# Performance work log

Hardware: AMD Instinct MI355X
Metric: run time of the kernel (lower is better)

## Reference

```python
import jax, jax.numpy as jnp
import numpy as np

B, Q, C = 8, 100, 1024
H, W = 64, 64
NH = 16
HD = C // NH
SCALE = HD ** -0.5
LN_EPS = 1e-5


def setup_inputs() -> dict:
    key = jax.random.key(0)
    ks = jax.random.split(key, 8)
    xav = lambda k, shp: jax.random.normal(k, shp, jnp.float32) * (2.0 / (shp[0] + shp[-1])) ** 0.5
    return {
        "tgt": jax.random.normal(ks[0], (B, Q, C), jnp.float32),
        "memory": jax.random.normal(ks[1], (B, H, W, C), jnp.float32),
        "memory_pos_emb": jax.random.normal(ks[2], (B, H, W, C), jnp.float32),
        "query_pos_emb": jax.random.normal(ks[3], (B, Q, C), jnp.float32),
        "Wq": xav(ks[4], (C, C)),
        "Wk": xav(ks[5], (C, C)),
        "Wv": xav(ks[6], (C, C)),
        "Wo": xav(ks[7], (C, C)),
        "bo": jnp.zeros((C,), jnp.float32),
        "ln_gamma": jnp.ones((C,), jnp.float32),
        "ln_beta": jnp.zeros((C,), jnp.float32),
    }


def _layernorm(x, g, b):
    mu = jnp.mean(x, axis=-1, keepdims=True)
    var = jnp.var(x, axis=-1, keepdims=True)
    return (x - mu) * jax.lax.rsqrt(var + LN_EPS) * g + b


def reference(tgt, memory, memory_pos_emb, query_pos_emb, Wq, Wk, Wv, Wo, bo, ln_gamma, ln_beta):
    # flatten spatial dims: [B,H,W,C] -> [B,K,C]
    mem = memory.reshape(B, H * W, C)
    mpos = memory_pos_emb.reshape(B, H * W, C)
    q_in = tgt + query_pos_emb          # [B,Q,C]
    k_in = mem + mpos                    # [B,K,C]
    # projections (torch Linear: x @ W.T), split heads -> [B,nh,*,hd]
    q = (q_in @ Wq.T).reshape(B, Q, NH, HD).transpose(0, 2, 1, 3)
    k = (k_in @ Wk.T).reshape(B, -1, NH, HD).transpose(0, 2, 1, 3)
    v = (mem @ Wv.T).reshape(B, -1, NH, HD).transpose(0, 2, 1, 3)
    dots = jnp.einsum('bhid,bhjd->bhij', q, k) * SCALE   # [B,nh,Q,K]
    # slot attention: softmax over QUERY axis, then renormalize over keys
    attn = jax.nn.softmax(dots, axis=2)
    attn = attn / (jnp.sum(attn, axis=-1, keepdims=True) + 1e-8)
    updates = jnp.einsum('bhij,bhjd->bhid', attn, v)     # [B,nh,Q,hd]
    updates = updates.transpose(0, 2, 1, 3).reshape(B, Q, C)
    out = updates @ Wo.T + bo
    # residual (dropout is identity in eval) + post-LayerNorm
    return _layernorm(tgt + out, ln_gamma, ln_beta)
```

## Files before the change

kernel.cpp:

```cpp
#include <hip/hip_runtime.h>

typedef unsigned short u16;
typedef __attribute__((ext_vector_type(8))) short bf16x8;
typedef __attribute__((ext_vector_type(4))) short bf16x4;
typedef __attribute__((ext_vector_type(4))) float f32x4;
typedef __attribute__((ext_vector_type(4))) unsigned short u16x4;
typedef __attribute__((ext_vector_type(8))) unsigned short u16x8;
typedef __attribute__((ext_vector_type(4))) int i32x4;
typedef __attribute__((ext_vector_type(4))) float f4;

#define DI __device__ __forceinline__


DI u16 f2bf(float f){
  unsigned int u = __float_as_uint(f);
  return (u16)((u + 0x7FFFu + ((u >> 16) & 1u)) >> 16);
}

DI void gl_lds16(const void* g, void* l){
  __builtin_amdgcn_global_load_lds((const __attribute__((address_space(1))) unsigned int*)g,
                                   (__attribute__((address_space(3))) unsigned int*)l, 16, 0, 0);
}

__global__ __launch_bounds__(256) void prep_kv(const float* __restrict__ mem,
                                               const float* __restrict__ mpos,
                                               u16* __restrict__ kA, u16* __restrict__ vA){
  const int t = blockIdx.x * 256 + threadIdx.x;
  #pragma unroll
  for (int i = 0; i < 4; ++i){
    const size_t g = (size_t)t + (size_t)i * 1048576;
    f4 m0 = __builtin_nontemporal_load((const f4*)mem  + g * 2);
    f4 m1 = __builtin_nontemporal_load((const f4*)mem  + g * 2 + 1);
    f4 p0 = __builtin_nontemporal_load((const f4*)mpos + g * 2);
    f4 p1 = __builtin_nontemporal_load((const f4*)mpos + g * 2 + 1);
    u16x8 k, v;
    #pragma unroll
    for (int j = 0; j < 4; ++j){
      k[j]     = f2bf(m0[j] + p0[j]);  v[j]     = f2bf(m0[j]);
      k[j + 4] = f2bf(m1[j] + p1[j]);  v[j + 4] = f2bf(m1[j]);
    }
    ((u16x8*)kA)[g] = k;
    ((u16x8*)vA)[g] = v;
  }
}

__global__ __launch_bounds__(256) void prep_qw(const float* __restrict__ tgt,
                                               const float* __restrict__ qpos,
                                               const float* __restrict__ Wq, const float* __restrict__ Wk,
                                               const float* __restrict__ Wv, const float* __restrict__ Wo,
                                               u16* __restrict__ qA, u16* __restrict__ Wbf){
  int gid = blockIdx.x * 256 + threadIdx.x;
  const int NQ4 = 819200 / 4;
  if (gid < NQ4){
    f4 a = ((const f4*)tgt)[gid];
    f4 b = ((const f4*)qpos)[gid];
    u16x4 r;
    #pragma unroll
    for (int j = 0; j < 4; ++j) r[j] = f2bf(a[j] + b[j]);
    ((u16x4*)qA)[gid] = r;
  } else {
    int wid = gid - NQ4;
    int sel = wid >> 18;
    int off = wid & 262143;
    const float* W = (sel == 0) ? Wq : (sel == 1) ? Wk : (sel == 2) ? Wv : Wo;
    f4 w = ((const f4*)W)[off];
    u16x4 r;
    #pragma unroll
    for (int j = 0; j < 4; ++j) r[j] = f2bf(w[j]);
    ((u16x4*)(Wbf))[(size_t)sel * 262144 + off] = r;
  }
}

__global__ __launch_bounds__(512, 1) void gemm256(
    const u16* __restrict__ A, const u16* __restrict__ Bw,
    u16* __restrict__ Cb, float scale)
{
  __shared__ __align__(16) char lds[131072];
  const int tid = threadIdx.x;
  const int l = tid & 63, w = tid >> 6;
  const int nwg = gridDim.x;
  const int sbid = (blockIdx.x & 7) * (nwg >> 3) + (blockIdx.x >> 3);
  const int mb = sbid >> 2, nb = sbid & 3;
  const int m0 = mb * 256, n0 = nb * 256;
  const int fr = l & 15, fg = l >> 4;
  const int wm = w >> 2, wn = w & 3;

  char* ldsA  = lds + wm * 8192 + l * 16;
  char* ldsB  = lds + 32768 + wn * 4096 + l * 16;
  char* ldsS0 = lds + w * 1024;
  char* ldsS1 = lds + (8 + w) * 1024;
  const u16* gA0 = A  + (size_t)(m0 + w * 16 + fr) * 1024 + fg * 8;
  const u16* gA1 = A  + (size_t)(m0 + (8 + w) * 16 + fr) * 1024 + fg * 8;
  const u16* gB0 = Bw + (size_t)(n0 + w * 16 + fr) * 1024 + fg * 8;
  const u16* gB1 = Bw + (size_t)(n0 + (8 + w) * 16 + fr) * 1024 + fg * 8;

  auto stA = [&](int pp, int kh, int kt){
    const int o = kt * 64 + kh * 32;
    gl_lds16(gA0 + o, ldsS0 + pp * 65536 + kh * 16384);
    gl_lds16(gA1 + o, ldsS1 + pp * 65536 + kh * 16384);
  };
  auto stB = [&](int pp, int kh, int kt){
    const int o = kt * 64 + kh * 32;
    gl_lds16(gB0 + o, ldsS0 + pp * 65536 + 32768 + kh * 16384);
    gl_lds16(gB1 + o, ldsS1 + pp * 65536 + 32768 + kh * 16384);
  };
  auto rdA4 = [&](bf16x8* av, int pp, int kh, int mfb){
    #pragma unroll
    for (int i = 0; i < 4; ++i)
      av[i] = *(const bf16x8*)(ldsA + pp * 65536 + kh * 16384 + (mfb + i) * 1024);
  };
  auto rdB4 = [&](bf16x8* bv, int pp, int kh){
    #pragma unroll
    for (int i = 0; i < 4; ++i)
      bv[i] = *(const bf16x8*)(ldsB + pp * 65536 + kh * 16384 + i * 1024);
  };

  f32x4 acc[8][4] = {};

  stA(0, 0, 0); stB(0, 0, 0); stA(0, 1, 0); stB(0, 1, 0);
  stA(1, 0, 1); stB(1, 0, 1);
  asm volatile("s_waitcnt vmcnt(8)" ::: "memory");
  __builtin_amdgcn_s_barrier();

  auto ktbody = [&](int P, int kt){
    const int kt1 = (kt + 1 > 15) ? 15 : kt + 1;
    const int kt2 = (kt + 2 > 15) ? 15 : kt + 2;
    bf16x8 av[4], bv[4];

    rdA4(av, P, 0, 0); rdB4(bv, P, 0);
    stA(P ^ 1, 1, kt1);
    __builtin_amdgcn_s_barrier();
    __builtin_amdgcn_s_setprio(1);
    #pragma unroll
    for (int i = 0; i < 4; ++i)
      #pragma unroll
      for (int n = 0; n < 4; ++n)
        acc[i][n] = __builtin_amdgcn_mfma_f32_16x16x32_bf16(av[i], bv[n], acc[i][n], 0, 0, 0);
    __builtin_amdgcn_s_setprio(0);
    __builtin_amdgcn_s_barrier();

    rdA4(av, P, 0, 4);
    stB(P ^ 1, 1, kt1);
    asm volatile("s_waitcnt vmcnt(8)" ::: "memory");
    __builtin_amdgcn_s_barrier();
    __builtin_amdgcn_s_setprio(1);
    #pragma unroll
    for (int i = 0; i < 4; ++i)
      #pragma unroll
      for (int n = 0; n < 4; ++n)
        acc[4 + i][n] = __builtin_amdgcn_mfma_f32_16x16x32_bf16(av[i], bv[n], acc[4 + i][n], 0, 0, 0);
    __builtin_amdgcn_s_setprio(0);
    __builtin_amdgcn_s_barrier();

    rdA4(av, P, 1, 0); rdB4(bv, P, 1);
    stA(P, 0, kt2);
    __builtin_amdgcn_s_barrier();
    __builtin_amdgcn_s_setprio(1);
    #pragma unroll
    for (int i = 0; i < 4; ++i)
      #pragma unroll
      for (int n = 0; n < 4; ++n)
        acc[i][n] = __builtin_amdgcn_mfma_f32_16x16x32_bf16(av[i], bv[n], acc[i][n], 0, 0, 0);
    __builtin_amdgcn_s_setprio(0);
    __builtin_amdgcn_s_barrier();

    rdA4(av, P, 1, 4);
    stB(P, 0, kt2);
    asm volatile("s_waitcnt vmcnt(8)" ::: "memory");
    __builtin_amdgcn_s_barrier();
    __builtin_amdgcn_s_setprio(1);
    #pragma unroll
    for (int i = 0; i < 4; ++i)
      #pragma unroll
      for (int n = 0; n < 4; ++n)
        acc[4 + i][n] = __builtin_amdgcn_mfma_f32_16x16x32_bf16(av[i], bv[n], acc[4 + i][n], 0, 0, 0);
    __builtin_amdgcn_s_setprio(0);
    __builtin_amdgcn_s_barrier();
  };

  for (int kk = 0; kk < 8; ++kk){
    ktbody(0, 2 * kk);
    ktbody(1, 2 * kk + 1);
  }

  asm volatile("s_waitcnt vmcnt(0)" ::: "memory");

  #pragma unroll
  for (int mf = 0; mf < 8; ++mf){
    #pragma unroll
    for (int nf = 0; nf < 4; ++nf){
      const int gcol = n0 + wn * 64 + nf * 16 + fr;
      #pragma unroll
      for (int r = 0; r < 4; ++r){
        const int grow = m0 + wm * 128 + mf * 16 + fg * 4 + r;
        Cb[(size_t)grow * 1024 + gcol] = f2bf(acc[mf][nf][r] * scale);
      }
    }
  }
}

template<int MODE>
__global__ __launch_bounds__(256, 2) void gemm_bt(
    const u16* __restrict__ A, const u16* __restrict__ Bw,
    u16* __restrict__ Cb, float* __restrict__ Cf,
    const float* __restrict__ bias, const float* __restrict__ resid,
    int M, float scale)
{
  __shared__ u16 lA[2][128 * 32];
  __shared__ u16 lB[2][128 * 32];
  const int tid = threadIdx.x;
  const int l = tid & 63, w = tid >> 6;
  const int nwg = gridDim.x;
  int bid = blockIdx.x;
  bid = (bid & 7) * (nwg >> 3) + (bid >> 3);
  const int mb = bid >> 3, nb = bid & 7;
  const int m0 = mb * 128, n0 = nb * 128;
  const int fr = l & 15, fg = l >> 4;
  const int wr = w >> 1, wc = w & 1;

  f32x4 acc[4][4] = {};

  auto stage = [&](int buf, int kt){
    const int k0 = kt * 32;
    #pragma unroll
    for (int q = 0; q < 2; ++q){
      int r = w * 32 + q * 16 + (l >> 2);
      int ar = m0 + r; if (ar >= M) ar = M - 1;
      gl_lds16(A  + (size_t)ar * 1024 + k0 + (l & 3) * 8, &lA[buf][(w * 32 + q * 16) * 32]);
      gl_lds16(Bw + (size_t)(n0 + r) * 1024 + k0 + (l & 3) * 8, &lB[buf][(w * 32 + q * 16) * 32]);
    }
  };

  stage(0, 0);
  __syncthreads();
  for (int kt = 0; kt < 32; ++kt){
    const int cur = kt & 1;
    if (kt < 31) stage(cur ^ 1, kt + 1);
    bf16x8 av[4], bv[4];
    #pragma unroll
    for (int m = 0; m < 4; ++m)
      av[m] = *(const bf16x8*)&lA[cur][(wr * 64 + m * 16 + fr) * 32 + fg * 8];
    #pragma unroll
    for (int n = 0; n < 4; ++n)
      bv[n] = *(const bf16x8*)&lB[cur][(wc * 64 + n * 16 + fr) * 32 + fg * 8];
    #pragma unroll
    for (int m = 0; m < 4; ++m)
      #pragma unroll
      for (int n = 0; n < 4; ++n)
        acc[m][n] = __builtin_amdgcn_mfma_f32_16x16x32_bf16(av[m], bv[n], acc[m][n], 0, 0, 0);
    __syncthreads();
  }

  #pragma unroll
  for (int m = 0; m < 4; ++m){
    const int grow_base = m0 + wr * 64 + m * 16 + fg * 4;
    #pragma unroll
    for (int n = 0; n < 4; ++n){
      const int gcol = n0 + wc * 64 + n * 16 + fr;
      #pragma unroll
      for (int r = 0; r < 4; ++r){
        const int grow = grow_base + r;
        if (grow < M){
          const float v = acc[m][n][r];
          if (MODE == 0) Cb[(size_t)grow * 1024 + gcol] = f2bf(v * scale);
          else           Cf[(size_t)grow * 1024 + gcol] = v + bias[gcol] + resid[(size_t)grow * 1024 + gcol];
        }
      }
    }
  }
}

__global__ __launch_bounds__(64, 1) void attn_k(
    const u16* __restrict__ qp, const u16* __restrict__ kp, const u16* __restrict__ vp,
    float* __restrict__ updpart, float* __restrict__ rspart)
{
  const int bidx = blockIdx.x;
  const int c = bidx & 7, h = (bidx >> 3) & 15, b = bidx >> 7;
  const int bh = b * 16 + h;
  const int l = threadIdx.x;
  const int fr = l & 15, fg = l >> 4;

  __shared__ u16 qlds[112 * 64];
  __shared__ __align__(16) u16 vlds[2][16 * 64];

  for (int t = 0; t < 14; ++t){
    int chunk = t * 64 + l;
    int row = chunk >> 3, cb = chunk & 7;
    i32x4 val = {0, 0, 0, 0};
    if (row < 100)
      val = *(const i32x4*)(qp + (size_t)(b * 100 + row) * 1024 + h * 64 + cb * 8);
    *(i32x4*)((char*)qlds + row * 128 + ((cb ^ (row & 7)) * 16)) = val;
  }
  __syncthreads();

  bf16x8 qf[7][2];
  #pragma unroll
  for (int n = 0; n < 7; ++n)
    #pragma unroll
    for (int ks = 0; ks < 2; ++ks){
      int row = n * 16 + fr;
      int cb = ks * 4 + fg;
      qf[n][ks] = *(const bf16x8*)((const char*)qlds + row * 128 + ((cb ^ (row & 7)) * 16));
    }

  f32x4 acc[7][4] = {};
  float rs[7] = {};
  const f32x4 fz = {0.f, 0.f, 0.f, 0.f};
  const size_t kvbase = ((size_t)b * 4096) * 1024 + h * 64;
  const int j00 = c * 512;

  const u16* ksrc = kp + kvbase + (size_t)fr * 1024 + fg * 8;
  const u16* vsrc = vp + kvbase + (size_t)(l >> 3) * 1024 + (l & 7) * 8;

  auto loadK = [&](int t, bf16x8& k0, bf16x8& k1){
    const size_t ro = (size_t)(j00 + t * 16) * 1024;
    k0 = *(const bf16x8*)(ksrc + ro);
    k1 = *(const bf16x8*)(ksrc + ro + 32);
  };
  auto loadV = [&](int t, bf16x8& a, bf16x8& bb){
    const size_t ro = (size_t)(j00 + t * 16) * 1024;
    a  = *(const bf16x8*)(vsrc + ro);
    bb = *(const bf16x8*)(vsrc + ro + 8 * 1024);
  };
  auto writeV = [&](int buf, bf16x8 a, bf16x8 bb){
    *(bf16x8*)&vlds[buf][l * 8] = a;
    *(bf16x8*)&vlds[buf][512 + l * 8] = bb;
  };

  bf16x8 kc0, kc1, kn0, kn1, vn0, vn1;
  loadK(0, kc0, kc1);
  loadV(0, vn0, vn1);
  writeV(0, vn0, vn1);

  for (int t = 0; t < 32; ++t){
    const int cur = t & 1;
    if (t < 31){
      loadK(t + 1, kn0, kn1);
      loadV(t + 1, vn0, vn1);
    }

    f32x4 s[7];
    #pragma unroll
    for (int n = 0; n < 7; ++n){
      s[n] = __builtin_amdgcn_mfma_f32_16x16x32_bf16(kc0, qf[n][0], fz, 0, 0, 0);
      s[n] = __builtin_amdgcn_mfma_f32_16x16x32_bf16(kc1, qf[n][1], s[n], 0, 0, 0);
    }
    if (fr >= 4){ s[6][0] = -1e30f; s[6][1] = -1e30f; s[6][2] = -1e30f; s[6][3] = -1e30f; }

    float pv[7][4];
    #pragma unroll
    for (int r = 0; r < 4; ++r){
      float m = s[0][r];
      #pragma unroll
      for (int n = 1; n < 7; ++n) m = fmaxf(m, s[n][r]);
      m = fmaxf(m, __shfl_xor(m, 1)); m = fmaxf(m, __shfl_xor(m, 2));
      m = fmaxf(m, __shfl_xor(m, 4)); m = fmaxf(m, __shfl_xor(m, 8));
      float sum = 0.f;
      #pragma unroll
      for (int n = 0; n < 7; ++n){ float e = __expf(s[n][r] - m); pv[n][r] = e; sum += e; }
      sum += __shfl_xor(sum, 1); sum += __shfl_xor(sum, 2);
      sum += __shfl_xor(sum, 4); sum += __shfl_xor(sum, 8);
      float inv = 1.0f / sum;
      #pragma unroll
      for (int n = 0; n < 7; ++n) pv[n][r] *= inv;
    }

    bf16x4 pk[7];
    #pragma unroll
    for (int n = 0; n < 7; ++n){
      rs[n] += pv[n][0] + pv[n][1] + pv[n][2] + pv[n][3];
      bf16x4 t4;
      t4[0] = (short)f2bf(pv[n][0]); t4[1] = (short)f2bf(pv[n][1]);
      t4[2] = (short)f2bf(pv[n][2]); t4[3] = (short)f2bf(pv[n][3]);
      pk[n] = t4;
    }

    bf16x4 vf[4];
    #pragma unroll
    for (int dt = 0; dt < 4; ++dt){
      bf16x4 tv;
      #pragma unroll
      for (int jj = 0; jj < 4; ++jj)
        tv[jj] = (short)vlds[cur][(fg * 4 + jj) * 64 + dt * 16 + fr];
      vf[dt] = tv;
    }

    #pragma unroll
    for (int n = 0; n < 7; ++n)
      #pragma unroll
      for (int dt = 0; dt < 4; ++dt)
        acc[n][dt] = __builtin_amdgcn_mfma_f32_16x16x16bf16_1k(vf[dt], pk[n], acc[n][dt], 0, 0, 0);

    if (t < 31){
      writeV(cur ^ 1, vn0, vn1);
      kc0 = kn0; kc1 = kn1;
    }
  }

  #pragma unroll
  for (int n = 0; n < 7; ++n){
    float v = rs[n];
    v += __shfl_xor(v, 16); v += __shfl_xor(v, 32);
    if (l < 16) rspart[((size_t)c * 128 + bh) * 112 + n * 16 + l] = v;
  }
  float* ub = updpart + ((size_t)c * 128 + bh) * 64 * 112;
  #pragma unroll
  for (int n = 0; n < 7; ++n)
    #pragma unroll
    for (int dt = 0; dt < 4; ++dt)
      #pragma unroll
      for (int r = 0; r < 4; ++r){
        int d = dt * 16 + fg * 4 + r;
        int i = n * 16 + fr;
        ub[d * 112 + i] = acc[n][dt][r];
      }
}

__global__ __launch_bounds__(128) void nrm_k(const float* __restrict__ updpart,
                                             const float* __restrict__ rspart,
                                             u16* __restrict__ updn){
  const int bid = blockIdx.x;
  const int d = bid & 63, h = (bid >> 6) & 15, b = bid >> 10;
  const int bh = b * 16 + h;
  const int tid = threadIdx.x;
  const int i = (tid < 112) ? tid : 111;
  float sum = 0.f, rsum = 0.f;
  #pragma unroll
  for (int cc = 0; cc < 8; ++cc){
    sum  += updpart[(((size_t)cc * 128 + bh) * 64 + d) * 112 + i];
    rsum += rspart[((size_t)cc * 128 + bh) * 112 + i];
  }
  if (tid < 100)
    updn[((size_t)b * 100 + tid) * 1024 + h * 64 + d] = f2bf(sum / (rsum + 1e-8f));
}

__global__ __launch_bounds__(256) void ln_k(const float* __restrict__ x,
                                            const float* __restrict__ g,
                                            const float* __restrict__ be,
                                            float* __restrict__ out){
  const int row = blockIdx.x;
  const int tid = threadIdx.x;
  const f4 xv = *(const f4*)(x + (size_t)row * 1024 + tid * 4);
  float s = xv[0] + xv[1] + xv[2] + xv[3];
  float q = xv[0]*xv[0] + xv[1]*xv[1] + xv[2]*xv[2] + xv[3]*xv[3];
  #pragma unroll
  for (int m = 1; m < 64; m <<= 1){ s += __shfl_xor(s, m); q += __shfl_xor(q, m); }
  __shared__ float ss[4], qq[4];
  const int w = tid >> 6;
  if ((tid & 63) == 0){ ss[w] = s; qq[w] = q; }
  __syncthreads();
  s = ss[0] + ss[1] + ss[2] + ss[3];
  q = qq[0] + qq[1] + qq[2] + qq[3];
  const float mu = s * (1.0f / 1024.0f);
  const float var = q * (1.0f / 1024.0f) - mu * mu;
  const float rstd = rsqrtf(var + 1e-5f);
  const f4 gv = *(const f4*)(g + tid * 4);
  const f4 bv = *(const f4*)(be + tid * 4);
  f4 o;
  #pragma unroll
  for (int j = 0; j < 4; ++j) o[j] = (xv[j] - mu) * rstd * gv[j] + bv[j];
  *(f4*)(out + (size_t)row * 1024 + tid * 4) = o;
}

extern "C" void kernel_launch(void* const* d_in, const int* in_sizes, int n_in,
                              void* d_out, int out_size, void* d_ws, size_t ws_size,
                              hipStream_t stream)
{
  const float* tgt   = (const float*)d_in[0];
  const float* mem   = (const float*)d_in[1];
  const float* mpos  = (const float*)d_in[2];
  const float* qpos  = (const float*)d_in[3];
  const float* Wq    = (const float*)d_in[4];
  const float* Wk    = (const float*)d_in[5];
  const float* Wv    = (const float*)d_in[6];
  const float* Wo    = (const float*)d_in[7];
  const float* bo    = (const float*)d_in[8];
  const float* gamma = (const float*)d_in[9];
  const float* beta  = (const float*)d_in[10];

  char* ws = (char*)d_ws;
  u16* qA     = (u16*)(ws + 0);
  u16* Wbf    = (u16*)(ws + 1638400);
  u16* kA     = (u16*)(ws + 10027008);
  u16* vA     = (u16*)(ws + 77135872);
  u16* qproj  = (u16*)(ws + 144244736);
  u16* kproj  = (u16*)(ws + 145883136);
  u16* vproj  = kA;
  float* updpart = (float*)(ws + 77135872);
  float* rspart  = (float*)(ws + 77135872 + 29360128);
  u16*   updn    = (u16*)  (ws + 77135872 + 29818880);
  float* resid   = (float*)(ws + 77135872 + 31457280);

  prep_kv<<<4096, 256, 0, stream>>>(mem, mpos, kA, vA);
  prep_qw<<<4896, 256, 0, stream>>>(tgt, qpos, Wq, Wk, Wv, Wo, qA, Wbf);
  gemm_bt<0><<<56,  256, 0, stream>>>(qA, Wbf, qproj, nullptr, nullptr, nullptr, 800, 0.125f);
  gemm256<<<512, 512, 0, stream>>>(kA, Wbf + 1048576, kproj, 1.0f);
  gemm256<<<512, 512, 0, stream>>>(vA, Wbf + 2097152, vproj, 1.0f);
  attn_k<<<1024, 64, 0, stream>>>(qproj, kproj, vproj, updpart, rspart);
  nrm_k<<<8192, 128, 0, stream>>>(updpart, rspart, updn);
  gemm_bt<1><<<56, 256, 0, stream>>>(updn, Wbf + 3145728, nullptr, resid, bo, tgt, 800, 1.0f);
  ln_k<<<800, 256, 0, stream>>>(resid, gamma, beta, (float*)d_out);
}
```

Measured before the change: 369.7 us.

## Merge K/V projection GEMMs into one launch and split attention keys across two waves

```diff
diff --git a/kernel.cpp b/kernel.cpp
--- a/kernel.cpp
+++ b/kernel.cpp
@@ -71,15 +71,10 @@
   }
 }
 
-__global__ __launch_bounds__(512, 1) void gemm256(
-    const u16* __restrict__ A, const u16* __restrict__ Bw,
-    u16* __restrict__ Cb, float scale)
+DI void gemm256_body(const u16* __restrict__ A, const u16* __restrict__ Bw,
+                     u16* __restrict__ Cb, float scale, int sbid, int tid, char* lds)
 {
-  __shared__ __align__(16) char lds[131072];
-  const int tid = threadIdx.x;
   const int l = tid & 63, w = tid >> 6;
-  const int nwg = gridDim.x;
-  const int sbid = (blockIdx.x & 7) * (nwg >> 3) + (blockIdx.x >> 3);
   const int mb = sbid >> 2, nb = sbid & 3;
   const int m0 = mb * 256, n0 = nb * 256;
   const int fr = l & 15, fg = l >> 4;
@@ -197,6 +192,27 @@
       }
     }
   }
+}
+
+__global__ __launch_bounds__(512, 1) void gemm256(
+    const u16* __restrict__ A, const u16* __restrict__ Bw, u16* __restrict__ Cb)
+{
+  __shared__ __align__(16) char lds[131072];
+  const int nwg = gridDim.x;
+  const int sbid = (blockIdx.x & 7) * (nwg >> 3) + (blockIdx.x >> 3);
+  gemm256_body(A, Bw, Cb, 1.0f, sbid, threadIdx.x, lds);
+}
+
+__global__ __launch_bounds__(512, 1) void gemm256kv(
+    const u16* __restrict__ A0, const u16* __restrict__ B0, u16* __restrict__ C0,
+    const u16* __restrict__ A1, const u16* __restrict__ B1, u16* __restrict__ C1)
+{
+  __shared__ __align__(16) char lds[131072];
+  const int sel = blockIdx.x >> 9;
+  const int inner = blockIdx.x & 511;
+  const int sbid = (inner & 7) * 64 + (inner >> 3);
+  if (sel == 0) gemm256_body(A0, B0, C0, 1.0f, sbid, threadIdx.x, lds);
+  else          gemm256_body(A1, B1, C1, 1.0f, sbid, threadIdx.x, lds);
 }
 
 template<int MODE>
@@ -270,21 +286,25 @@
   }
 }
 
-__global__ __launch_bounds__(64, 1) void attn_k(
+__global__ __launch_bounds__(128, 1) void attn_k(
     const u16* __restrict__ qp, const u16* __restrict__ kp, const u16* __restrict__ vp,
     float* __restrict__ updpart, float* __restrict__ rspart)
 {
   const int bidx = blockIdx.x;
   const int c = bidx & 7, h = (bidx >> 3) & 15, b = bidx >> 7;
   const int bh = b * 16 + h;
-  const int l = threadIdx.x;
+  const int tid = threadIdx.x;
+  const int w = tid >> 6, l = tid & 63;
   const int fr = l & 15, fg = l >> 4;
 
-  __shared__ u16 qlds[112 * 64];
-  __shared__ __align__(16) u16 vlds[2][16 * 64];
-
-  for (int t = 0; t < 14; ++t){
-    int chunk = t * 64 + l;
+  __shared__ __align__(16) char smem[36864];
+  u16*   qlds   = (u16*)smem;
+  f32x4* mrgacc = (f32x4*)smem;
+  u16*   vlds   = (u16*)(smem + 28672);
+  float* mrgrs  = (float*)(smem + 28672);
+
+  for (int t = 0; t < 7; ++t){
+    int chunk = t * 128 + tid;
     int row = chunk >> 3, cb = chunk & 7;
     i32x4 val = {0, 0, 0, 0};
     if (row < 100)
@@ -311,6 +331,7 @@
 
   const u16* ksrc = kp + kvbase + (size_t)fr * 1024 + fg * 8;
   const u16* vsrc = vp + kvbase + (size_t)(l >> 3) * 1024 + (l & 7) * 8;
+  u16* myvlds = vlds + w * 2048;
 
   auto loadK = [&](int t, bf16x8& k0, bf16x8& k1){
     const size_t ro = (size_t)(j00 + t * 16) * 1024;
@@ -323,20 +344,21 @@
     bb = *(const bf16x8*)(vsrc + ro + 8 * 1024);
   };
   auto writeV = [&](int buf, bf16x8 a, bf16x8 bb){
-    *(bf16x8*)&vlds[buf][l * 8] = a;
-    *(bf16x8*)&vlds[buf][512 + l * 8] = bb;
+    *(bf16x8*)&myvlds[buf * 1024 + l * 8] = a;
+    *(bf16x8*)&myvlds[buf * 1024 + 512 + l * 8] = bb;
   };
 
   bf16x8 kc0, kc1, kn0, kn1, vn0, vn1;
-  loadK(0, kc0, kc1);
-  loadV(0, vn0, vn1);
+  loadK(w, kc0, kc1);
+  loadV(w, vn0, vn1);
   writeV(0, vn0, vn1);
 
-  for (int t = 0; t < 32; ++t){
-    const int cur = t & 1;
-    if (t < 31){
-      loadK(t + 1, kn0, kn1);
-      loadV(t + 1, vn0, vn1);
+  for (int tt = 0; tt < 16; ++tt){
+    const int t = 2 * tt + w;
+    const int cur = tt & 1;
+    if (tt < 15){
+      loadK(t + 2, kn0, kn1);
+      loadV(t + 2, vn0, vn1);
     }
 
     f32x4 s[7];
@@ -381,7 +403,7 @@
       bf16x4 tv;
       #pragma unroll
       for (int jj = 0; jj < 4; ++jj)
-        tv[jj] = (short)vlds[cur][(fg * 4 + jj) * 64 + dt * 16 + fr];
+        tv[jj] = (short)myvlds[cur * 1024 + (fg * 4 + jj) * 64 + dt * 16 + fr];
       vf[dt] = tv;
     }
 
@@ -391,29 +413,53 @@
       for (int dt = 0; dt < 4; ++dt)
         acc[n][dt] = __builtin_amdgcn_mfma_f32_16x16x16bf16_1k(vf[dt], pk[n], acc[n][dt], 0, 0, 0);
 
-    if (t < 31){
+    if (tt < 15){
       writeV(cur ^ 1, vn0, vn1);
       kc0 = kn0; kc1 = kn1;
     }
   }
 
+  float rv[7];
   #pragma unroll
   for (int n = 0; n < 7; ++n){
     float v = rs[n];
     v += __shfl_xor(v, 16); v += __shfl_xor(v, 32);
-    if (l < 16) rspart[((size_t)c * 128 + bh) * 112 + n * 16 + l] = v;
-  }
-  float* ub = updpart + ((size_t)c * 128 + bh) * 64 * 112;
-  #pragma unroll
-  for (int n = 0; n < 7; ++n)
-    #pragma unroll
-    for (int dt = 0; dt < 4; ++dt)
-      #pragma unroll
-      for (int r = 0; r < 4; ++r){
-        int d = dt * 16 + fg * 4 + r;
-        int i = n * 16 + fr;
-        ub[d * 112 + i] = acc[n][dt][r];
-      }
+    rv[n] = v;
+  }
+
+  __syncthreads();
+  if (w == 1){
+    #pragma unroll
+    for (int n = 0; n < 7; ++n)
+      #pragma unroll
+      for (int dt = 0; dt < 4; ++dt)
+        mrgacc[(n * 4 + dt) * 64 + l] = acc[n][dt];
+    #pragma unroll
+    for (int n = 0; n < 7; ++n)
+      if (l < 16) mrgrs[n * 16 + l] = rv[n];
+  }
+  __syncthreads();
+  if (w == 0){
+    #pragma unroll
+    for (int n = 0; n < 7; ++n)
+      #pragma unroll
+      for (int dt = 0; dt < 4; ++dt)
+        acc[n][dt] += mrgacc[(n * 4 + dt) * 64 + l];
+    #pragma unroll
+    for (int n = 0; n < 7; ++n)
+      if (l < 16) rspart[((size_t)c * 128 + bh) * 112 + n * 16 + l] = rv[n] + mrgrs[n * 16 + l];
+    float* ub = updpart + ((size_t)c * 128 + bh) * 64 * 112;
+    #pragma unroll
+    for (int n = 0; n < 7; ++n)
+      #pragma unroll
+      for (int dt = 0; dt < 4; ++dt)
+        #pragma unroll
+        for (int r = 0; r < 4; ++r){
+          int d = dt * 16 + fg * 4 + r;
+          int i = n * 16 + fr;
+          ub[d * 112 + i] = acc[n][dt][r];
+        }
+  }
 }
 
 __global__ __launch_bounds__(128) void nrm_k(const float* __restrict__ updpart,
@@ -485,7 +531,6 @@
   u16* vA     = (u16*)(ws + 77135872);
   u16* qproj  = (u16*)(ws + 144244736);
   u16* kproj  = (u16*)(ws + 145883136);
-  u16* vproj  = kA;
   float* updpart = (float*)(ws + 77135872);
   float* rspart  = (float*)(ws + 77135872 + 29360128);
   u16*   updn    = (u16*)  (ws + 77135872 + 29818880);
@@ -493,10 +538,19 @@
 
   prep_kv<<<4096, 256, 0, stream>>>(mem, mpos, kA, vA);
   prep_qw<<<4896, 256, 0, stream>>>(tgt, qpos, Wq, Wk, Wv, Wo, qA, Wbf);
-  gemm_bt<0><<<56,  256, 0, stream>>>(qA, Wbf, qproj, nullptr, nullptr, nullptr, 800, 0.125f);
-  gemm256<<<512, 512, 0, stream>>>(kA, Wbf + 1048576, kproj, 1.0f);
-  gemm256<<<512, 512, 0, stream>>>(vA, Wbf + 2097152, vproj, 1.0f);
-  attn_k<<<1024, 64, 0, stream>>>(qproj, kproj, vproj, updpart, rspart);
+  gemm_bt<0><<<56, 256, 0, stream>>>(qA, Wbf, qproj, nullptr, nullptr, nullptr, 800, 0.125f);
+
+  u16* vproj;
+  if (ws_size >= (size_t)212992000 + 67108864){
+    vproj = (u16*)(ws + 212992000);
+    gemm256kv<<<1024, 512, 0, stream>>>(kA, Wbf + 1048576, kproj, vA, Wbf + 2097152, vproj);
+  } else {
+    vproj = kA;
+    gemm256<<<512, 512, 0, stream>>>(kA, Wbf + 1048576, kproj);
+    gemm256<<<512, 512, 0, stream>>>(vA, Wbf + 2097152, vproj);
+  }
+
+  attn_k<<<1024, 128, 0, stream>>>(qproj, kproj, vproj, updpart, rspart);
   nrm_k<<<8192, 128, 0, stream>>>(updpart, rspart, updn);
   gemm_bt<1><<<56, 256, 0, stream>>>(updn, Wbf + 3145728, nullptr, resid, bo, tgt, 800, 1.0f);
   ln_k<<<800, 256, 0, stream>>>(resid, gamma, beta, (float*)d_out);
```

New measurement: 387.6 us. +4.8%, slower.
